# Kernel optimization log

Hardware: AMD Instinct MI355X
Metric: run time of the kernel (lower is better)

## Reference

```python
import jax, jax.numpy as jnp
import numpy as np

B, T, H = 32, 2048, 1024


def setup_inputs() -> dict:
    key = jax.random.key(0)
    ks = jax.random.split(key, 5)
    s = 1.0 / np.sqrt(H)
    return {
        "x": jax.random.normal(ks[0], (B, H), dtype=jnp.float32),
        "context": jax.random.normal(ks[1], (B, T, H), dtype=jnp.float32),
        "mask": jnp.ones((B, T), dtype=bool),
        "Wq": jax.random.normal(ks[2], (H, H), dtype=jnp.float32) * s,
        "bq": jnp.zeros((H,), dtype=jnp.float32),
        "Wm": jax.random.normal(ks[3], (H, H), dtype=jnp.float32) * s,
        "bm": jnp.zeros((H,), dtype=jnp.float32),
        "v": jax.random.normal(ks[4], (H,), dtype=jnp.float32) * s,
    }


def reference(x, context, mask, Wq, bq, Wm, bm, v):
    # h_x: [B,1,H]; h_c: [B,T,H]  (mask is unused, matching the original module)
    h_x = (x @ Wq.T + bq)[:, None, :]
    h_c = jnp.einsum('bth,oh->bto', context, Wm) + bm
    # score: [B,T] = tanh(h_x + h_c) . v, then softmax over T
    score = jax.nn.softmax(jnp.einsum('bth,h->bt', jnp.tanh(h_x + h_c), v), axis=-1)
    # context-weighted sum over T -> [B,H]
    c = jnp.einsum('bth,bt->bh', context, score)
    return (c, score)
```

## Files before the change

kernel.cpp:

```cpp
#include <hip/hip_runtime.h>
#include <math.h>

#define B_ 32
#define T_ 2048
#define H_ 1024

typedef __bf16 bf16x8 __attribute__((ext_vector_type(8)));
typedef float f32x4 __attribute__((ext_vector_type(4)));

__device__ __forceinline__ unsigned short f2bf(float f) {
  unsigned int u = __float_as_uint(f);
  u += 0x7fffu + ((u >> 16) & 1u);
  return (unsigned short)(u >> 16);
}

__device__ __forceinline__ float bf2f(unsigned short s) {
  return __uint_as_float(((unsigned int)s) << 16);
}

__device__ __forceinline__ float fast_tanh(float x) {
  float e = __expf(2.0f * x);
  return 1.0f - __fdividef(2.0f, e + 1.0f);
}

__global__ void prep_kernel(const float* __restrict__ x, const float* __restrict__ Wq,
                            const float* __restrict__ bq, const float* __restrict__ bm,
                            const float* __restrict__ Wm, const float* __restrict__ ctx,
                            float* __restrict__ hxb, unsigned short* __restrict__ wmb,
                            unsigned short* __restrict__ ctxb) {
  int blk = blockIdx.x, tid = threadIdx.x;
  if (blk < 128) {
    int idx = (blk << 8) + tid;
    int b = idx >> 10, o = idx & (H_ - 1);
    const float4* xr = (const float4*)(x + b * H_);
    const float4* wr = (const float4*)(Wq + o * H_);
    float s = 0.f;
#pragma unroll 8
    for (int h = 0; h < H_ / 4; ++h) {
      float4 xv = xr[h], wv = wr[h];
      s += xv.x * wv.x + xv.y * wv.y + xv.z * wv.z + xv.w * wv.w;
    }
    hxb[idx] = s + bq[o] + bm[o];
  } else if (blk < 1152) {
    int i = ((blk - 128) << 10) + (tid << 2);
    float4 wv = *(const float4*)(Wm + i);
    *(ushort4*)(wmb + i) = make_ushort4(f2bf(wv.x), f2bf(wv.y), f2bf(wv.z), f2bf(wv.w));
  } else {
    size_t i = ((size_t)(blk - 1152) << 11) + ((size_t)tid << 3);
    float4 a = *(const float4*)(ctx + i);
    float4 c = *(const float4*)(ctx + i + 4);
    *(ushort4*)(ctxb + i) = make_ushort4(f2bf(a.x), f2bf(a.y), f2bf(a.z), f2bf(a.w));
    *(ushort4*)(ctxb + i + 4) = make_ushort4(f2bf(c.x), f2bf(c.y), f2bf(c.z), f2bf(c.w));
  }
}

template <bool PRECONV>
__global__ __launch_bounds__(256) void score_kernel(
    const float* __restrict__ ctxf, const unsigned short* __restrict__ ctxb,
    const unsigned short* __restrict__ wmb,
    const float* __restrict__ hxb, const float* __restrict__ v,
    float* __restrict__ logits) {
  __shared__ __align__(16) unsigned short As[128][72];
  __shared__ float part[128];

  int tid = threadIdx.x;
  int blk = blockIdx.x;
  int b = blk >> 4;
  int t0 = (blk & 15) << 7;
  if (tid < 128) part[tid] = 0.f;

  int lane = tid & 63;
  int wave = tid >> 6;
  int wm = (wave >> 1) << 6;
  int wn = (wave & 1) << 6;
  int q = lane >> 4;
  int m = lane & 15;
  const unsigned short* cb = PRECONV ? (ctxb + ((size_t)b * T_ + t0) * H_) : nullptr;
  const float* cf = PRECONV ? nullptr : (ctxf + ((size_t)b * T_ + t0) * H_);

  int ar = tid >> 3;
  int ac = (tid & 7) << 3;

  for (int ot = 0; ot < 8; ++ot) {
    int o0 = ot << 7;
    f32x4 acc[4][4];
#pragma unroll
    for (int i = 0; i < 4; ++i)
#pragma unroll
      for (int j = 0; j < 4; ++j) acc[i][j] = (f32x4){0.f, 0.f, 0.f, 0.f};

    for (int k0 = 0; k0 < H_; k0 += 64) {
      __syncthreads();
#pragma unroll
      for (int rep = 0; rep < 4; ++rep) {
        int row = ar + (rep << 5);
        if (PRECONV) {
          *(uint4*)(&As[row][ac]) = *(const uint4*)(cb + (size_t)row * H_ + k0 + ac);
        } else {
          const float* src = cf + (size_t)row * H_ + k0 + ac;
          float4 f0 = *(const float4*)(src);
          float4 f1 = *(const float4*)(src + 4);
          *(ushort4*)(&As[row][ac]) =
              make_ushort4(f2bf(f0.x), f2bf(f0.y), f2bf(f0.z), f2bf(f0.w));
          *(ushort4*)(&As[row][ac + 4]) =
              make_ushort4(f2bf(f1.x), f2bf(f1.y), f2bf(f1.z), f2bf(f1.w));
        }
      }
      __syncthreads();
#pragma unroll
      for (int kk = 0; kk < 2; ++kk) {
        bf16x8 af[4], bfr[4];
        const unsigned short* wp =
            wmb + (size_t)(o0 + wn + m) * H_ + k0 + (kk << 5) + (q << 3);
#pragma unroll
        for (int j = 0; j < 4; ++j)
          bfr[j] = *(const bf16x8*)(wp + ((size_t)(j << 4) * H_));
#pragma unroll
        for (int i = 0; i < 4; ++i)
          af[i] = *(const bf16x8*)(&As[wm + (i << 4) + m][(kk << 5) + (q << 3)]);
#pragma unroll
        for (int i = 0; i < 4; ++i)
#pragma unroll
          for (int j = 0; j < 4; ++j)
            acc[i][j] = __builtin_amdgcn_mfma_f32_16x16x32_bf16(af[i], bfr[j], acc[i][j], 0, 0, 0);
      }
    }

    float hb[4], vv[4];
#pragma unroll
    for (int j = 0; j < 4; ++j) {
      int o = o0 + wn + (j << 4) + m;
      hb[j] = hxb[(b << 10) + o];
      vv[j] = v[o];
    }
#pragma unroll
    for (int i = 0; i < 4; ++i) {
#pragma unroll
      for (int r = 0; r < 4; ++r) {
        float s = 0.f;
#pragma unroll
        for (int j = 0; j < 4; ++j) s += fast_tanh(acc[i][j][r] + hb[j]) * vv[j];
        s += __shfl_xor(s, 1);
        s += __shfl_xor(s, 2);
        s += __shfl_xor(s, 4);
        s += __shfl_xor(s, 8);
        if (m == 0) atomicAdd(&part[wm + (i << 4) + (q << 2) + r], s);
      }
    }
  }
  __syncthreads();
  if (tid < 128) logits[b * T_ + t0 + tid] = part[tid];
}

__global__ void softmax_kernel(const float* __restrict__ logits, float* __restrict__ score) {
  int b = blockIdx.x, tid = threadIdx.x;
  __shared__ float wmax[4], wsum[4];
  const float* lb = logits + b * T_;
  float l[8];
  float mx = -3.4e38f;
#pragma unroll
  for (int i = 0; i < 8; ++i) { l[i] = lb[tid + (i << 8)]; mx = fmaxf(mx, l[i]); }
#pragma unroll
  for (int d = 1; d < 64; d <<= 1) mx = fmaxf(mx, __shfl_xor(mx, d));
  if ((tid & 63) == 0) wmax[tid >> 6] = mx;
  __syncthreads();
  mx = fmaxf(fmaxf(wmax[0], wmax[1]), fmaxf(wmax[2], wmax[3]));
  float e[8];
  float se = 0.f;
#pragma unroll
  for (int i = 0; i < 8; ++i) { e[i] = __expf(l[i] - mx); se += e[i]; }
#pragma unroll
  for (int d = 1; d < 64; d <<= 1) se += __shfl_xor(se, d);
  if ((tid & 63) == 0) wsum[tid >> 6] = se;
  __syncthreads();
  se = wsum[0] + wsum[1] + wsum[2] + wsum[3];
  float inv = 1.0f / se;
#pragma unroll
  for (int i = 0; i < 8; ++i) score[b * T_ + tid + (i << 8)] = e[i] * inv;
}

template <bool PRECONV>
__global__ void wsum_kernel(const float* __restrict__ ctxf, const unsigned short* __restrict__ ctxb,
                            const float* __restrict__ score, float* __restrict__ outc) {
  int tid = threadIdx.x;
  int h = (blockIdx.x << 9) + (tid << 1);
  int tch = blockIdx.y << 8;
  int b = blockIdx.z;
  __shared__ float sc[256];
  sc[tid] = score[b * T_ + tch + tid];
  __syncthreads();
  float s0 = 0.f, s1 = 0.f;
  if (PRECONV) {
    const unsigned short* cp = ctxb + ((size_t)b * T_ + tch) * H_ + h;
#pragma unroll 4
    for (int t = 0; t < 256; ++t) {
      unsigned int u = *(const unsigned int*)(cp + (size_t)t * H_);
      s0 += bf2f((unsigned short)(u & 0xffffu)) * sc[t];
      s1 += bf2f((unsigned short)(u >> 16)) * sc[t];
    }
  } else {
    const float* cp = ctxf + ((size_t)b * T_ + tch) * H_ + h;
#pragma unroll 4
    for (int t = 0; t < 256; ++t) {
      float2 f = *(const float2*)(cp + (size_t)t * H_);
      s0 += f.x * sc[t];
      s1 += f.y * sc[t];
    }
  }
  atomicAdd(&outc[(b << 10) + h], s0);
  atomicAdd(&outc[(b << 10) + h + 1], s1);
}

extern "C" void kernel_launch(void* const* d_in, const int* in_sizes, int n_in,
                              void* d_out, int out_size, void* d_ws, size_t ws_size,
                              hipStream_t stream) {
  const float* x   = (const float*)d_in[0];
  const float* ctx = (const float*)d_in[1];
  const float* Wq  = (const float*)d_in[3];
  const float* bq  = (const float*)d_in[4];
  const float* Wm  = (const float*)d_in[5];
  const float* bm  = (const float*)d_in[6];
  const float* v   = (const float*)d_in[7];

  float* out_c = (float*)d_out;
  float* out_s = out_c + B_ * H_;

  char* ws = (char*)d_ws;
  float* hxb = (float*)ws;
  unsigned short* wmb = (unsigned short*)(ws + 131072);
  float* logits = (float*)(ws + 131072 + 2097152);
  size_t off_ctxb = 131072 + 2097152 + 262144;
  unsigned short* ctxb = (unsigned short*)(ws + off_ctxb);
  size_t need = off_ctxb + (size_t)B_ * T_ * H_ * 2;
  bool preconv = (ws_size >= need);

  hipMemsetAsync(out_c, 0, B_ * H_ * sizeof(float), stream);
  int prep_blocks = preconv ? (1152 + 32768) : 1152;
  prep_kernel<<<dim3(prep_blocks), 256, 0, stream>>>(x, Wq, bq, bm, Wm, ctx, hxb, wmb,
                                                     preconv ? ctxb : nullptr);
  if (preconv) {
    score_kernel<true><<<dim3(512), 256, 0, stream>>>(ctx, ctxb, wmb, hxb, v, logits);
  } else {
    score_kernel<false><<<dim3(512), 256, 0, stream>>>(ctx, ctxb, wmb, hxb, v, logits);
  }
  softmax_kernel<<<dim3(B_), 256, 0, stream>>>(logits, out_s);
  if (preconv) {
    wsum_kernel<true><<<dim3(H_ / 512, T_ / 256, B_), 256, 0, stream>>>(ctx, ctxb, out_s, out_c);
  } else {
    wsum_kernel<false><<<dim3(H_ / 512, T_ / 256, B_), 256, 0, stream>>>(ctx, ctxb, out_s, out_c);
  }
}
```

Baseline: 753.0 us.

## Split score GEMM across output tiles with atomic logits and fuse softmax into wsum

The score kernel now takes one 128-wide output tile per block instead of looping over all eight, so the grid grows from 512 to 4096 blocks. Partial logits are combined with global atomicAdd into a buffer that the prep kernel zeroes, and that kernel also zeroes out_c, replacing the memset. The softmax kernel is removed: each wsum block recomputes its batch row's softmax from the logits, and only one block per batch writes the score output. This aims to fill the GPU during the score GEMM and cut launches, at the cost of global atomics, nondeterministic summation order and repeated softmax work.

```diff
diff --git a/kernel.cpp b/kernel.cpp
--- a/kernel.cpp
+++ b/kernel.cpp
@@ -27,7 +27,8 @@
                             const float* __restrict__ bq, const float* __restrict__ bm,
                             const float* __restrict__ Wm, const float* __restrict__ ctx,
                             float* __restrict__ hxb, unsigned short* __restrict__ wmb,
-                            unsigned short* __restrict__ ctxb) {
+                            unsigned short* __restrict__ ctxb,
+                            float* __restrict__ logits, float* __restrict__ outc) {
   int blk = blockIdx.x, tid = threadIdx.x;
   if (blk < 128) {
     int idx = (blk << 8) + tid;
@@ -45,8 +46,15 @@
     int i = ((blk - 128) << 10) + (tid << 2);
     float4 wv = *(const float4*)(Wm + i);
     *(ushort4*)(wmb + i) = make_ushort4(f2bf(wv.x), f2bf(wv.y), f2bf(wv.z), f2bf(wv.w));
+  } else if (blk < 1248) {
+    int zblk = blk - 1152;
+    if (zblk < 64) {
+      *(float4*)(logits + (zblk << 10) + (tid << 2)) = (float4){0.f, 0.f, 0.f, 0.f};
+    } else {
+      *(float4*)(outc + ((zblk - 64) << 10) + (tid << 2)) = (float4){0.f, 0.f, 0.f, 0.f};
+    }
   } else {
-    size_t i = ((size_t)(blk - 1152) << 11) + ((size_t)tid << 3);
+    size_t i = ((size_t)(blk - 1248) << 11) + ((size_t)tid << 3);
     float4 a = *(const float4*)(ctx + i);
     float4 c = *(const float4*)(ctx + i + 4);
     *(ushort4*)(ctxb + i) = make_ushort4(f2bf(a.x), f2bf(a.y), f2bf(a.z), f2bf(a.w));
@@ -59,14 +67,17 @@
     const float* __restrict__ ctxf, const unsigned short* __restrict__ ctxb,
     const unsigned short* __restrict__ wmb,
     const float* __restrict__ hxb, const float* __restrict__ v,
-    float* __restrict__ logits) {
+    float* logits) {
   __shared__ __align__(16) unsigned short As[128][72];
   __shared__ float part[128];
 
   int tid = threadIdx.x;
-  int blk = blockIdx.x;
-  int b = blk >> 4;
-  int t0 = (blk & 15) << 7;
+  int xx = blockIdx.x;
+  int ot = xx >> 9;
+  int bt = xx & 511;
+  int b = bt >> 4;
+  int t0 = (bt & 15) << 7;
+  int o0 = ot << 7;
   if (tid < 128) part[tid] = 0.f;
 
   int lane = tid & 63;
@@ -81,80 +92,84 @@
   int ar = tid >> 3;
   int ac = (tid & 7) << 3;
 
-  for (int ot = 0; ot < 8; ++ot) {
-    int o0 = ot << 7;
-    f32x4 acc[4][4];
-#pragma unroll
-    for (int i = 0; i < 4; ++i)
-#pragma unroll
-      for (int j = 0; j < 4; ++j) acc[i][j] = (f32x4){0.f, 0.f, 0.f, 0.f};
-
-    for (int k0 = 0; k0 < H_; k0 += 64) {
-      __syncthreads();
-#pragma unroll
-      for (int rep = 0; rep < 4; ++rep) {
-        int row = ar + (rep << 5);
-        if (PRECONV) {
-          *(uint4*)(&As[row][ac]) = *(const uint4*)(cb + (size_t)row * H_ + k0 + ac);
-        } else {
-          const float* src = cf + (size_t)row * H_ + k0 + ac;
-          float4 f0 = *(const float4*)(src);
-          float4 f1 = *(const float4*)(src + 4);
-          *(ushort4*)(&As[row][ac]) =
-              make_ushort4(f2bf(f0.x), f2bf(f0.y), f2bf(f0.z), f2bf(f0.w));
-          *(ushort4*)(&As[row][ac + 4]) =
-              make_ushort4(f2bf(f1.x), f2bf(f1.y), f2bf(f1.z), f2bf(f1.w));
-        }
+  f32x4 acc[4][4];
+#pragma unroll
+  for (int i = 0; i < 4; ++i)
+#pragma unroll
+    for (int j = 0; j < 4; ++j) acc[i][j] = (f32x4){0.f, 0.f, 0.f, 0.f};
+
+  for (int k0 = 0; k0 < H_; k0 += 64) {
+    __syncthreads();
+#pragma unroll
+    for (int rep = 0; rep < 4; ++rep) {
+      int row = ar + (rep << 5);
+      if (PRECONV) {
+        *(uint4*)(&As[row][ac]) = *(const uint4*)(cb + (size_t)row * H_ + k0 + ac);
+      } else {
+        const float* src = cf + (size_t)row * H_ + k0 + ac;
+        float4 f0 = *(const float4*)(src);
+        float4 f1 = *(const float4*)(src + 4);
+        *(ushort4*)(&As[row][ac]) =
+            make_ushort4(f2bf(f0.x), f2bf(f0.y), f2bf(f0.z), f2bf(f0.w));
+        *(ushort4*)(&As[row][ac + 4]) =
+            make_ushort4(f2bf(f1.x), f2bf(f1.y), f2bf(f1.z), f2bf(f1.w));
       }
-      __syncthreads();
-#pragma unroll
-      for (int kk = 0; kk < 2; ++kk) {
-        bf16x8 af[4], bfr[4];
-        const unsigned short* wp =
-            wmb + (size_t)(o0 + wn + m) * H_ + k0 + (kk << 5) + (q << 3);
+    }
+    __syncthreads();
+#pragma unroll
+    for (int kk = 0; kk < 2; ++kk) {
+      bf16x8 af[4], bfr[4];
+      const unsigned short* wp =
+          wmb + (size_t)(o0 + wn + m) * H_ + k0 + (kk << 5) + (q << 3);
+#pragma unroll
+      for (int j = 0; j < 4; ++j)
+        bfr[j] = *(const bf16x8*)(wp + ((size_t)(j << 4) * H_));
+#pragma unroll
+      for (int i = 0; i < 4; ++i)
+        af[i] = *(const bf16x8*)(&As[wm + (i << 4) + m][(kk << 5) + (q << 3)]);
+#pragma unroll
+      for (int i = 0; i < 4; ++i)
 #pragma unroll
         for (int j = 0; j < 4; ++j)
-          bfr[j] = *(const bf16x8*)(wp + ((size_t)(j << 4) * H_));
-#pragma unroll
-        for (int i = 0; i < 4; ++i)
-          af[i] = *(const bf16x8*)(&As[wm + (i << 4) + m][(kk << 5) + (q << 3)]);
-#pragma unroll
-        for (int i = 0; i < 4; ++i)
-#pragma unroll
-          for (int j = 0; j < 4; ++j)
-            acc[i][j] = __builtin_amdgcn_mfma_f32_16x16x32_bf16(af[i], bfr[j], acc[i][j], 0, 0, 0);
-      }
-    }
-
-    float hb[4], vv[4];
-#pragma unroll
-    for (int j = 0; j < 4; ++j) {
-      int o = o0 + wn + (j << 4) + m;
-      hb[j] = hxb[(b << 10) + o];
-      vv[j] = v[o];
-    }
-#pragma unroll
-    for (int i = 0; i < 4; ++i) {
-#pragma unroll
-      for (int r = 0; r < 4; ++r) {
-        float s = 0.f;
-#pragma unroll
-        for (int j = 0; j < 4; ++j) s += fast_tanh(acc[i][j][r] + hb[j]) * vv[j];
-        s += __shfl_xor(s, 1);
-        s += __shfl_xor(s, 2);
-        s += __shfl_xor(s, 4);
-        s += __shfl_xor(s, 8);
-        if (m == 0) atomicAdd(&part[wm + (i << 4) + (q << 2) + r], s);
-      }
-    }
-  }
-  __syncthreads();
-  if (tid < 128) logits[b * T_ + t0 + tid] = part[tid];
-}
-
-__global__ void softmax_kernel(const float* __restrict__ logits, float* __restrict__ score) {
-  int b = blockIdx.x, tid = threadIdx.x;
-  __shared__ float wmax[4], wsum[4];
+          acc[i][j] = __builtin_amdgcn_mfma_f32_16x16x32_bf16(af[i], bfr[j], acc[i][j], 0, 0, 0);
+    }
+  }
+
+  float hb[4], vv[4];
+#pragma unroll
+  for (int j = 0; j < 4; ++j) {
+    int o = o0 + wn + (j << 4) + m;
+    hb[j] = hxb[(b << 10) + o];
+    vv[j] = v[o];
+  }
+#pragma unroll
+  for (int i = 0; i < 4; ++i) {
+#pragma unroll
+    for (int r = 0; r < 4; ++r) {
+      float s = 0.f;
+#pragma unroll
+      for (int j = 0; j < 4; ++j) s += fast_tanh(acc[i][j][r] + hb[j]) * vv[j];
+      s += __shfl_xor(s, 1);
+      s += __shfl_xor(s, 2);
+      s += __shfl_xor(s, 4);
+      s += __shfl_xor(s, 8);
+      if (m == 0) atomicAdd(&part[wm + (i << 4) + (q << 2) + r], s);
+    }
+  }
+  __syncthreads();
+  if (tid < 128) atomicAdd(&logits[b * T_ + t0 + tid], part[tid]);
+}
+
+template <bool PRECONV>
+__global__ void wsum_kernel(const float* __restrict__ ctxf, const unsigned short* __restrict__ ctxb,
+                            const float* __restrict__ logits,
+                            float* __restrict__ score, float* __restrict__ outc) {
+  int tid = threadIdx.x;
+  int b = blockIdx.z;
+  int tch = blockIdx.y << 8;
+  __shared__ float wred[4];
+  __shared__ float sc[256];
+
   const float* lb = logits + b * T_;
   float l[8];
   float mx = -3.4e38f;
@@ -162,33 +177,28 @@
   for (int i = 0; i < 8; ++i) { l[i] = lb[tid + (i << 8)]; mx = fmaxf(mx, l[i]); }
 #pragma unroll
   for (int d = 1; d < 64; d <<= 1) mx = fmaxf(mx, __shfl_xor(mx, d));
-  if ((tid & 63) == 0) wmax[tid >> 6] = mx;
-  __syncthreads();
-  mx = fmaxf(fmaxf(wmax[0], wmax[1]), fmaxf(wmax[2], wmax[3]));
+  if ((tid & 63) == 0) wred[tid >> 6] = mx;
+  __syncthreads();
+  mx = fmaxf(fmaxf(wred[0], wred[1]), fmaxf(wred[2], wred[3]));
+  __syncthreads();
   float e[8];
   float se = 0.f;
 #pragma unroll
   for (int i = 0; i < 8; ++i) { e[i] = __expf(l[i] - mx); se += e[i]; }
 #pragma unroll
   for (int d = 1; d < 64; d <<= 1) se += __shfl_xor(se, d);
-  if ((tid & 63) == 0) wsum[tid >> 6] = se;
-  __syncthreads();
-  se = wsum[0] + wsum[1] + wsum[2] + wsum[3];
+  if ((tid & 63) == 0) wred[tid >> 6] = se;
+  __syncthreads();
+  se = wred[0] + wred[1] + wred[2] + wred[3];
   float inv = 1.0f / se;
-#pragma unroll
-  for (int i = 0; i < 8; ++i) score[b * T_ + tid + (i << 8)] = e[i] * inv;
-}
-
-template <bool PRECONV>
-__global__ void wsum_kernel(const float* __restrict__ ctxf, const unsigned short* __restrict__ ctxb,
-                            const float* __restrict__ score, float* __restrict__ outc) {
-  int tid = threadIdx.x;
+  sc[tid] = e[blockIdx.y] * inv;
+  if (blockIdx.x == 0 && blockIdx.y == 0) {
+#pragma unroll
+    for (int i = 0; i < 8; ++i) score[b * T_ + tid + (i << 8)] = e[i] * inv;
+  }
+  __syncthreads();
+
   int h = (blockIdx.x << 9) + (tid << 1);
-  int tch = blockIdx.y << 8;
-  int b = blockIdx.z;
-  __shared__ float sc[256];
-  sc[tid] = score[b * T_ + tch + tid];
-  __syncthreads();
   float s0 = 0.f, s1 = 0.f;
   if (PRECONV) {
     const unsigned short* cp = ctxb + ((size_t)b * T_ + tch) * H_ + h;
@@ -234,19 +244,14 @@
   size_t need = off_ctxb + (size_t)B_ * T_ * H_ * 2;
   bool preconv = (ws_size >= need);
 
-  hipMemsetAsync(out_c, 0, B_ * H_ * sizeof(float), stream);
-  int prep_blocks = preconv ? (1152 + 32768) : 1152;
+  int prep_blocks = preconv ? (1248 + 32768) : 1248;
   prep_kernel<<<dim3(prep_blocks), 256, 0, stream>>>(x, Wq, bq, bm, Wm, ctx, hxb, wmb,
-                                                     preconv ? ctxb : nullptr);
+                                                     preconv ? ctxb : nullptr, logits, out_c);
   if (preconv) {
-    score_kernel<true><<<dim3(512), 256, 0, stream>>>(ctx, ctxb, wmb, hxb, v, logits);
+    score_kernel<true><<<dim3(4096), 256, 0, stream>>>(ctx, ctxb, wmb, hxb, v, logits);
+    wsum_kernel<true><<<dim3(H_ / 512, T_ / 256, B_), 256, 0, stream>>>(ctx, ctxb, logits, out_s, out_c);
   } else {
-    score_kernel<false><<<dim3(512), 256, 0, stream>>>(ctx, ctxb, wmb, hxb, v, logits);
-  }
-  softmax_kernel<<<dim3(B_), 256, 0, stream>>>(logits, out_s);
-  if (preconv) {
-    wsum_kernel<true><<<dim3(H_ / 512, T_ / 256, B_), 256, 0, stream>>>(ctx, ctxb, out_s, out_c);
-  } else {
-    wsum_kernel<false><<<dim3(H_ / 512, T_ / 256, B_), 256, 0, stream>>>(ctx, ctxb, out_s, out_c);
-  }
-}
+    score_kernel<false><<<dim3(4096), 256, 0, stream>>>(ctx, ctxb, wmb, hxb, v, logits);
+    wsum_kernel<false><<<dim3(H_ / 512, T_ / 256, B_), 256, 0, stream>>>(ctx, ctxb, logits, out_s, out_c);
+  }
+}
```

Result: no change. 767.0 us (+1.8%).
